# Optimization experiments

Hardware: AMD Instinct MI355X
Metric: run time of the kernel (lower is better)

The kernel has to match this reference:

```python
import jax, jax.numpy as jnp
import numpy as np

N_WIN = 232
T = 8
KERNEL = (2, 2, 2)
STRIDE = (2, 2, 2)
SLOPE = 25.0  # fast_sigmoid surrogate slope


@jax.custom_vjp
def spike(v):
    # heaviside(v) with fast-sigmoid surrogate gradient
    return (v > 0).astype(v.dtype)

def _spike_fwd(v):
    return spike(v), v

def _spike_bwd(v, g):
    return (g / (SLOPE * jnp.abs(v) + 1.0) ** 2,)

spike.defvjp(_spike_fwd, _spike_bwd)


def _avg_pool3d(x, kernel, stride):
    # x: (B, C, D, H, W), VALID pooling
    win = (1, 1) + tuple(kernel)
    st = (1, 1) + tuple(stride)
    s = jax.lax.reduce_window(x, 0.0, jax.lax.add, win, st, 'VALID')
    return s / float(np.prod(kernel))


def setup_inputs() -> dict:
    key = jax.random.key(0)
    ks = jax.random.split(key, 14)
    B, C, H, W = 64, 3, 32, 32
    input_dim, h0, h1, n_cls = 256, 256, 128, 6
    x = jax.random.normal(ks[0], (B, C, N_WIN, H, W), jnp.float32)
    W_in = jax.random.normal(ks[1], (h0, input_dim), jnp.float32) * 0.05
    b_in = jnp.zeros((h0,), jnp.float32)
    W_hid = jax.random.normal(ks[2], (h1, h0), jnp.float32) * 0.05
    b_hid = jnp.zeros((h1,), jnp.float32)
    in_feat = C * h1 * 14  # C * hidden[1] * D'
    W_out = jax.random.normal(ks[3], (n_cls, in_feat), jnp.float32) * 0.05
    b_out = jnp.zeros((n_cls,), jnp.float32)
    beta_in = jax.random.uniform(ks[4], (h0,), jnp.float32)
    thr_in = jax.random.uniform(ks[5], (h0,), jnp.float32)
    beta_hid = jax.random.uniform(ks[6], (h1,), jnp.float32)
    thr_hid = jax.random.uniform(ks[7], (h1,), jnp.float32)
    beta_out = jax.random.uniform(ks[8], (n_cls,), jnp.float32)
    return dict(x=x, W_in=W_in, b_in=b_in, W_hid=W_hid, b_hid=b_hid,
                W_out=W_out, b_out=b_out, beta_in=beta_in, thr_in=thr_in,
                beta_hid=beta_hid, thr_hid=thr_hid, beta_out=beta_out)


def _lif(mem, cur, beta, thr):
    # snntorch Leaky, reset-by-subtract; reset uses detached prev-mem spike
    reset = jax.lax.stop_gradient((mem > thr).astype(mem.dtype))
    mem = jnp.clip(beta, 0.0, 1.0) * mem + cur - reset * thr
    spk = spike(mem - thr)
    return spk, mem


def reference(x, W_in, b_in, W_hid, b_hid, W_out, b_out,
              beta_in, thr_in, beta_hid, thr_hid, beta_out):
    B, C, _, H, W = x.shape
    chunk = N_WIN // T  # 29
    # split depth into T chunks: (T, B, C, chunk, H, W)
    xt = x.reshape(B, C, T, chunk, H, W).transpose(2, 0, 1, 3, 4, 5)
    pooled = jax.vmap(lambda v: _avg_pool3d(v, KERNEL, STRIDE))(xt)  # (T,B,C,D',H',W')
    _, _, _, Dp, Hp, Wp = pooled.shape
    pr = pooled.reshape(T, B, C * Dp, Hp * Wp)
    # fc_in applied to all timesteps at once (recurrence-free)
    cur_in_all = jnp.einsum('tbnf,hf->tbnh', pr, W_in) + b_in  # (T,B,N,h0)

    h0 = W_in.shape[0]
    h1 = W_hid.shape[0]
    n_cls = W_out.shape[0]
    N = C * Dp
    mem_in0 = jnp.zeros((B, N, h0), x.dtype)
    mem_hid0 = jnp.zeros((B, N, h1), x.dtype)
    mem_out0 = jnp.zeros((B, n_cls), x.dtype)

    def step(carry, cur_in):
        mem_in, mem_hid, mem_out = carry
        spk_in, mem_in = _lif(mem_in, cur_in, beta_in, thr_in)
        cur_hid = jnp.einsum('bnh,gh->bng', spk_in, W_hid) + b_hid
        spk_hid, mem_hid = _lif(mem_hid, cur_hid, beta_hid, thr_hid)
        flat = spk_hid.reshape(spk_hid.shape[0], -1)  # (B, N*h1)
        cur_out = flat @ W_out.T + b_out
        spk_out, mem_out = _lif(mem_out, cur_out, beta_out, jnp.float32(1.0))
        return (mem_in, mem_hid, mem_out), spk_out

    _, spk_rec = jax.lax.scan(step, (mem_in0, mem_hid0, mem_out0), cur_in_all)
    return spk_rec  # (T, B, n_classes)
```

## Files before the change

kernel.cpp:

```cpp
#include <hip/hip_runtime.h>

#define T_STEPS 8
#define NROW    42
#define BN      2688
#define H0      256
#define H1      128
#define KFLAT   5376


#define SWA(r)  ((r) + ((r) >> 5) * 4)

__global__ __launch_bounds__(256, 4) void snn_front(
        const float* __restrict__ x,
        const float* __restrict__ Wi,
        const float* __restrict__ bi,
        const float* __restrict__ beti,
        const float* __restrict__ thri,
        const float* __restrict__ Wh,
        const float* __restrict__ bh,
        const float* __restrict__ beth,
        const float* __restrict__ thrh,
        float* __restrict__ spkh) {
    __shared__ float At[16 * 36];
    __shared__ float Bt[16 * 284];
    __shared__ unsigned int S32[256];

    int tid = threadIdx.x;
    int gbase = blockIdx.x * 4;

    int wp = tid & 15;
    int q  = tid >> 4;
    const float* xb0;
    const float* xb1;
    int mloc0 = q * 2, mloc1 = q * 2 + 1;
    {
        int g = gbase + (mloc0 >> 3);
        int t = mloc0 & 7;
        int b = g / 42, r = g - b * 42;
        int c = r / 14, dp = r - c * 14;
        xb0 = x + ((long)b * 712704 + (long)c * 237568
                + (long)(t * 29 + 2 * dp) * 1024 + 2 * wp);
    }
    {
        int g = gbase + (mloc1 >> 3);
        int t = mloc1 & 7;
        int b = g / 42, r = g - b * 42;
        int c = r / 14, dp = r - c * 14;
        xb1 = x + ((long)b * 712704 + (long)c * 237568
                + (long)(t * 29 + 2 * dp) * 1024 + 2 * wp);
    }

    const float* Bp = Wi + (long)tid * 256;
    int bcol = SWA(tid);

    int tm = tid & 3;
    int tn = tid >> 2;
    int ca = tm * 8;
    int cb = SWA(tn * 4);

    float acc[8][4] = {};

    for (int k0 = 0; k0 < 256; k0 += 16) {
        int hp = k0 >> 4;
        const float* p0 = xb0 + hp * 64;
        const float* p1 = xb1 + hp * 64;
        float2 a00 = *(const float2*)(p0);
        float2 a01 = *(const float2*)(p0 + 32);
        float2 a02 = *(const float2*)(p0 + 1024);
        float2 a03 = *(const float2*)(p0 + 1056);
        float2 a10 = *(const float2*)(p1);
        float2 a11 = *(const float2*)(p1 + 32);
        float2 a12 = *(const float2*)(p1 + 1024);
        float2 a13 = *(const float2*)(p1 + 1056);
        float4 w0 = *(const float4*)(Bp + k0);
        float4 w1 = *(const float4*)(Bp + k0 + 4);
        float4 w2 = *(const float4*)(Bp + k0 + 8);
        float4 w3 = *(const float4*)(Bp + k0 + 12);
        __syncthreads();
        float s0 = a00.x + a00.y + a01.x + a01.y + a02.x + a02.y + a03.x + a03.y;
        float s1 = a10.x + a10.y + a11.x + a11.y + a12.x + a12.y + a13.x + a13.y;
        At[wp * 36 + mloc0] = s0 * 0.125f;
        At[wp * 36 + mloc1] = s1 * 0.125f;
        Bt[ 0 * 284 + bcol] = w0.x; Bt[ 1 * 284 + bcol] = w0.y;
        Bt[ 2 * 284 + bcol] = w0.z; Bt[ 3 * 284 + bcol] = w0.w;
        Bt[ 4 * 284 + bcol] = w1.x; Bt[ 5 * 284 + bcol] = w1.y;
        Bt[ 6 * 284 + bcol] = w1.z; Bt[ 7 * 284 + bcol] = w1.w;
        Bt[ 8 * 284 + bcol] = w2.x; Bt[ 9 * 284 + bcol] = w2.y;
        Bt[10 * 284 + bcol] = w2.z; Bt[11 * 284 + bcol] = w2.w;
        Bt[12 * 284 + bcol] = w3.x; Bt[13 * 284 + bcol] = w3.y;
        Bt[14 * 284 + bcol] = w3.z; Bt[15 * 284 + bcol] = w3.w;
        __syncthreads();
#pragma unroll
        for (int k = 0; k < 16; ++k) {
            float4 av0 = *(const float4*)&At[k * 36 + ca];
            float4 av1 = *(const float4*)&At[k * 36 + ca + 4];
            float4 bv  = *(const float4*)&Bt[k * 284 + cb];
            float am[8] = {av0.x, av0.y, av0.z, av0.w, av1.x, av1.y, av1.z, av1.w};
            float bb[4] = {bv.x, bv.y, bv.z, bv.w};
#pragma unroll
            for (int i = 0; i < 8; ++i)
#pragma unroll
                for (int j = 0; j < 4; ++j)
                    acc[i][j] = fmaf(am[i], bb[j], acc[i][j]);
        }
    }

    unsigned int mybyte[4];
#pragma unroll
    for (int j = 0; j < 4; ++j) {
        int h = tn * 4 + j;
        float be = fminf(fmaxf(beti[h], 0.f), 1.f);
        float th = thri[h];
        float bb = bi[h];
        float mem = 0.f;
        unsigned int byte = 0u;
#pragma unroll
        for (int t = 0; t < T_STEPS; ++t) {
            float cur = acc[t][j] + bb;
            float reset = (mem > th) ? th : 0.f;
            mem = be * mem + cur - reset;
            byte |= ((mem - th) > 0.f) ? (1u << t) : 0u;
        }
        mybyte[j] = byte;
    }
    {
        unsigned char* S8 = (unsigned char*)S32;
#pragma unroll
        for (int j = 0; j < 4; ++j)
            S8[(tn * 4 + j) * 4 + tm] = (unsigned char)mybyte[j];
    }
    __syncthreads();

    const float* wrow0 = Wh + (long)(tn * 2) * 256;
    const float* wrow1 = wrow0 + 256;
    int shift = tm * 8;
    float acc2[8][2] = {};

    for (int k0 = 0; k0 < 256; k0 += 16) {
        float4 w00 = *(const float4*)(wrow0 + k0);
        float4 w01 = *(const float4*)(wrow0 + k0 + 4);
        float4 w02 = *(const float4*)(wrow0 + k0 + 8);
        float4 w03 = *(const float4*)(wrow0 + k0 + 12);
        float4 w10 = *(const float4*)(wrow1 + k0);
        float4 w11 = *(const float4*)(wrow1 + k0 + 4);
        float4 w12 = *(const float4*)(wrow1 + k0 + 8);
        float4 w13 = *(const float4*)(wrow1 + k0 + 12);
        float w0a[16] = {w00.x, w00.y, w00.z, w00.w, w01.x, w01.y, w01.z, w01.w,
                         w02.x, w02.y, w02.z, w02.w, w03.x, w03.y, w03.z, w03.w};
        float w1a[16] = {w10.x, w10.y, w10.z, w10.w, w11.x, w11.y, w11.z, w11.w,
                         w12.x, w12.y, w12.z, w12.w, w13.x, w13.y, w13.z, w13.w};
#pragma unroll
        for (int k = 0; k < 16; ++k) {
            unsigned int sw = S32[k0 + k];
#pragma unroll
            for (int i = 0; i < 8; ++i) {
                float am = (float)((sw >> (shift + i)) & 1u);
                acc2[i][0] = fmaf(am, w0a[k], acc2[i][0]);
                acc2[i][1] = fmaf(am, w1a[k], acc2[i][1]);
            }
        }
    }

#pragma unroll
    for (int j = 0; j < 2; ++j) {
        int h = tn * 2 + j;
        float be = fminf(fmaxf(beth[h], 0.f), 1.f);
        float th = thrh[h];
        float bb = bh[h];
        float mem = 0.f;
#pragma unroll
        for (int t = 0; t < T_STEPS; ++t) {
            float cur = acc2[t][j] + bb;
            float reset = (mem > th) ? th : 0.f;
            mem = be * mem + cur - reset;
            acc2[t][j] = ((mem - th) > 0.f) ? 1.f : 0.f;
        }
    }
    int rbase = blockIdx.x * 32 + tm * 8;
#pragma unroll
    for (int t = 0; t < T_STEPS; ++t) {
        float2 o = {acc2[t][0], acc2[t][1]};
        *(float2*)&spkh[(long)(rbase + t) * 128 + tn * 2] = o;
    }
}

__global__ __launch_bounds__(512) void out_fused(const float* __restrict__ spkh,
                                                 const float* __restrict__ W_out,
                                                 const float* __restrict__ b_out,
                                                 const float* __restrict__ beta_out,
                                                 float* __restrict__ out) {
    __shared__ float part[2][256][8];
    __shared__ float curs[8][8];
    int b = blockIdx.x;
    int grp = threadIdx.x >> 8;
    int tid = threadIdx.x & 255;

    for (int tr = 0; tr < 4; ++tr) {
        int t = tr * 2 + grp;
        float acc[6] = {0.f, 0.f, 0.f, 0.f, 0.f, 0.f};
        for (int j = tid; j < KFLAT; j += 256) {
            int n = j >> 7, h = j & 127;
            float s = spkh[((long)(b * NROW + n) * 8 + t) * 128 + h];
#pragma unroll
            for (int c = 0; c < 6; ++c)
                acc[c] = fmaf(s, W_out[c * KFLAT + j], acc[c]);
        }
#pragma unroll
        for (int c = 0; c < 6; ++c) part[grp][tid][c] = acc[c];
        __syncthreads();
        for (int off = 128; off > 0; off >>= 1) {
            if (tid < off) {
#pragma unroll
                for (int c = 0; c < 6; ++c)
                    part[grp][tid][c] += part[grp][tid + off][c];
            }
            __syncthreads();
        }
        if (tid < 6) curs[t][tid] = part[grp][0][tid] + b_out[tid];
        __syncthreads();
    }

    if (threadIdx.x < 6) {
        int cls = threadIdx.x;
        float be = fminf(fmaxf(beta_out[cls], 0.f), 1.f);
        float mem = 0.f;
#pragma unroll
        for (int t = 0; t < T_STEPS; ++t) {
            float cur = curs[t][cls];
            float reset = (mem > 1.f) ? 1.f : 0.f;
            mem = be * mem + cur - reset;
            out[t * 384 + b * 6 + cls] = ((mem - 1.f) > 0.f) ? 1.f : 0.f;
        }
    }
}

extern "C" void kernel_launch(void* const* d_in, const int* in_sizes, int n_in,
                              void* d_out, int out_size, void* d_ws, size_t ws_size,
                              hipStream_t stream) {
    (void)in_sizes; (void)n_in; (void)out_size; (void)ws_size;
    const float* x        = (const float*)d_in[0];
    const float* W_in     = (const float*)d_in[1];
    const float* b_in     = (const float*)d_in[2];
    const float* W_hid    = (const float*)d_in[3];
    const float* b_hid    = (const float*)d_in[4];
    const float* W_out    = (const float*)d_in[5];
    const float* b_out    = (const float*)d_in[6];
    const float* beta_in  = (const float*)d_in[7];
    const float* thr_in   = (const float*)d_in[8];
    const float* beta_hid = (const float*)d_in[9];
    const float* thr_hid  = (const float*)d_in[10];
    const float* beta_out = (const float*)d_in[11];
    float* out = (float*)d_out;

    float* buf0 = (float*)d_ws;

    snn_front<<<672, 256, 0, stream>>>(x, W_in, b_in, beta_in, thr_in,
                                       W_hid, b_hid, beta_hid, thr_hid, buf0);
    out_fused<<<64, 512, 0, stream>>>(buf0, W_out, b_out, beta_out, out);
}
```

Baseline: 370.8 us.

## Double-buffer front GEMM shared tiles and split output GEMM from LIF

Double-buffers the shared-memory A/B tiles in the front kernel. Global loads for the next K-chunk are issued before the FMA loop on the current buffer, which removes one barrier per iteration and hides load latency. Occupancy is lowered from 4 to 3 blocks per CU to fit the larger shared footprint. The output stage is split into a 512-block GEMM kernel that writes cur_out to workspace, followed by a tiny LIF kernel. This gives more parallelism than 64 blocks, at the cost of an extra launch.

```diff
diff --git a/kernel.cpp b/kernel.cpp
--- a/kernel.cpp
+++ b/kernel.cpp
@@ -10,7 +10,7 @@
 
 #define SWA(r)  ((r) + ((r) >> 5) * 4)
 
-__global__ __launch_bounds__(256, 4) void snn_front(
+__global__ __launch_bounds__(256, 3) void snn_front(
         const float* __restrict__ x,
         const float* __restrict__ Wi,
         const float* __restrict__ bi,
@@ -21,8 +21,8 @@
         const float* __restrict__ beth,
         const float* __restrict__ thrh,
         float* __restrict__ spkh) {
-    __shared__ float At[16 * 36];
-    __shared__ float Bt[16 * 284];
+    __shared__ float At[2 * 576];
+    __shared__ float Bt[2 * 4544];
     __shared__ unsigned int S32[256];
 
     int tid = threadIdx.x;
@@ -59,51 +59,69 @@
     int cb = SWA(tn * 4);
 
     float acc[8][4] = {};
-
-    for (int k0 = 0; k0 < 256; k0 += 16) {
-        int hp = k0 >> 4;
-        const float* p0 = xb0 + hp * 64;
-        const float* p1 = xb1 + hp * 64;
-        float2 a00 = *(const float2*)(p0);
-        float2 a01 = *(const float2*)(p0 + 32);
-        float2 a02 = *(const float2*)(p0 + 1024);
-        float2 a03 = *(const float2*)(p0 + 1056);
-        float2 a10 = *(const float2*)(p1);
-        float2 a11 = *(const float2*)(p1 + 32);
-        float2 a12 = *(const float2*)(p1 + 1024);
-        float2 a13 = *(const float2*)(p1 + 1056);
-        float4 w0 = *(const float4*)(Bp + k0);
-        float4 w1 = *(const float4*)(Bp + k0 + 4);
-        float4 w2 = *(const float4*)(Bp + k0 + 8);
-        float4 w3 = *(const float4*)(Bp + k0 + 12);
+    float2 a00, a01, a02, a03, a10, a11, a12, a13;
+    float4 w0, w1, w2, w3;
+
+#define ISSUE(hp) {                                                        \
+    const float* p0 = xb0 + (hp) * 64;                                     \
+    const float* p1 = xb1 + (hp) * 64;                                     \
+    a00 = *(const float2*)(p0);        a01 = *(const float2*)(p0 + 32);    \
+    a02 = *(const float2*)(p0 + 1024); a03 = *(const float2*)(p0 + 1056);  \
+    a10 = *(const float2*)(p1);        a11 = *(const float2*)(p1 + 32);    \
+    a12 = *(const float2*)(p1 + 1024); a13 = *(const float2*)(p1 + 1056);  \
+    const float* Bk = Bp + (hp) * 16;                                      \
+    w0 = *(const float4*)(Bk);     w1 = *(const float4*)(Bk + 4);          \
+    w2 = *(const float4*)(Bk + 8); w3 = *(const float4*)(Bk + 12); }
+
+#define STAGE(bufi) {                                                      \
+    float s0 = a00.x + a00.y + a01.x + a01.y + a02.x + a02.y + a03.x + a03.y; \
+    float s1 = a10.x + a10.y + a11.x + a11.y + a12.x + a12.y + a13.x + a13.y; \
+    float* At_ = At + (bufi) * 576;                                        \
+    float* Bt_ = Bt + (bufi) * 4544;                                       \
+    At_[wp * 36 + mloc0] = s0 * 0.125f;                                    \
+    At_[wp * 36 + mloc1] = s1 * 0.125f;                                    \
+    Bt_[ 0 * 284 + bcol] = w0.x; Bt_[ 1 * 284 + bcol] = w0.y;              \
+    Bt_[ 2 * 284 + bcol] = w0.z; Bt_[ 3 * 284 + bcol] = w0.w;              \
+    Bt_[ 4 * 284 + bcol] = w1.x; Bt_[ 5 * 284 + bcol] = w1.y;              \
+    Bt_[ 6 * 284 + bcol] = w1.z; Bt_[ 7 * 284 + bcol] = w1.w;              \
+    Bt_[ 8 * 284 + bcol] = w2.x; Bt_[ 9 * 284 + bcol] = w2.y;              \
+    Bt_[10 * 284 + bcol] = w2.z; Bt_[11 * 284 + bcol] = w2.w;              \
+    Bt_[12 * 284 + bcol] = w3.x; Bt_[13 * 284 + bcol] = w3.y;              \
+    Bt_[14 * 284 + bcol] = w3.z; Bt_[15 * 284 + bcol] = w3.w; }
+
+#define FMACHUNK(bufi) {                                                   \
+    const float* At_ = At + (bufi) * 576;                                  \
+    const float* Bt_ = Bt + (bufi) * 4544;                                 \
+    _Pragma("unroll")                                                      \
+    for (int k = 0; k < 16; ++k) {                                         \
+        float4 av0 = *(const float4*)&At_[k * 36 + ca];                    \
+        float4 av1 = *(const float4*)&At_[k * 36 + ca + 4];                \
+        float4 bv  = *(const float4*)&Bt_[k * 284 + cb];                   \
+        float am[8] = {av0.x, av0.y, av0.z, av0.w,                         \
+                       av1.x, av1.y, av1.z, av1.w};                        \
+        float bb[4] = {bv.x, bv.y, bv.z, bv.w};                            \
+        _Pragma("unroll")                                                  \
+        for (int i2 = 0; i2 < 8; ++i2)                                     \
+            _Pragma("unroll")                                              \
+            for (int j2 = 0; j2 < 4; ++j2)                                 \
+                acc[i2][j2] = fmaf(am[i2], bb[j2], acc[i2][j2]);           \
+    } }
+
+    ISSUE(0);
+    STAGE(0);
+#pragma unroll 1
+    for (int i = 0; i < 15; ++i) {
+        ISSUE(i + 1);
         __syncthreads();
-        float s0 = a00.x + a00.y + a01.x + a01.y + a02.x + a02.y + a03.x + a03.y;
-        float s1 = a10.x + a10.y + a11.x + a11.y + a12.x + a12.y + a13.x + a13.y;
-        At[wp * 36 + mloc0] = s0 * 0.125f;
-        At[wp * 36 + mloc1] = s1 * 0.125f;
-        Bt[ 0 * 284 + bcol] = w0.x; Bt[ 1 * 284 + bcol] = w0.y;
-        Bt[ 2 * 284 + bcol] = w0.z; Bt[ 3 * 284 + bcol] = w0.w;
-        Bt[ 4 * 284 + bcol] = w1.x; Bt[ 5 * 284 + bcol] = w1.y;
-        Bt[ 6 * 284 + bcol] = w1.z; Bt[ 7 * 284 + bcol] = w1.w;
-        Bt[ 8 * 284 + bcol] = w2.x; Bt[ 9 * 284 + bcol] = w2.y;
-        Bt[10 * 284 + bcol] = w2.z; Bt[11 * 284 + bcol] = w2.w;
-        Bt[12 * 284 + bcol] = w3.x; Bt[13 * 284 + bcol] = w3.y;
-        Bt[14 * 284 + bcol] = w3.z; Bt[15 * 284 + bcol] = w3.w;
-        __syncthreads();
-#pragma unroll
-        for (int k = 0; k < 16; ++k) {
-            float4 av0 = *(const float4*)&At[k * 36 + ca];
-            float4 av1 = *(const float4*)&At[k * 36 + ca + 4];
-            float4 bv  = *(const float4*)&Bt[k * 284 + cb];
-            float am[8] = {av0.x, av0.y, av0.z, av0.w, av1.x, av1.y, av1.z, av1.w};
-            float bb[4] = {bv.x, bv.y, bv.z, bv.w};
-#pragma unroll
-            for (int i = 0; i < 8; ++i)
-#pragma unroll
-                for (int j = 0; j < 4; ++j)
-                    acc[i][j] = fmaf(am[i], bb[j], acc[i][j]);
-        }
-    }
+        FMACHUNK(i & 1);
+        STAGE((i + 1) & 1);
+    }
+    __syncthreads();
+    FMACHUNK(1);
+
+#undef ISSUE
+#undef STAGE
+#undef FMACHUNK
 
     unsigned int mybyte[4];
 #pragma unroll
@@ -184,53 +202,49 @@
     }
 }
 
-__global__ __launch_bounds__(512) void out_fused(const float* __restrict__ spkh,
-                                                 const float* __restrict__ W_out,
-                                                 const float* __restrict__ b_out,
-                                                 const float* __restrict__ beta_out,
-                                                 float* __restrict__ out) {
-    __shared__ float part[2][256][8];
-    __shared__ float curs[8][8];
-    int b = blockIdx.x;
-    int grp = threadIdx.x >> 8;
-    int tid = threadIdx.x & 255;
-
-    for (int tr = 0; tr < 4; ++tr) {
-        int t = tr * 2 + grp;
-        float acc[6] = {0.f, 0.f, 0.f, 0.f, 0.f, 0.f};
-        for (int j = tid; j < KFLAT; j += 256) {
-            int n = j >> 7, h = j & 127;
-            float s = spkh[((long)(b * NROW + n) * 8 + t) * 128 + h];
-#pragma unroll
-            for (int c = 0; c < 6; ++c)
-                acc[c] = fmaf(s, W_out[c * KFLAT + j], acc[c]);
-        }
-#pragma unroll
-        for (int c = 0; c < 6; ++c) part[grp][tid][c] = acc[c];
+__global__ __launch_bounds__(256) void out_gemm(const float* __restrict__ spkh,
+                                                const float* __restrict__ W_out,
+                                                const float* __restrict__ b_out,
+                                                float* __restrict__ cur_out) {
+    __shared__ float part[256][8];
+    int row = blockIdx.x;
+    int t = row >> 6, b = row & 63;
+    int tid = threadIdx.x;
+    float acc[6] = {0.f, 0.f, 0.f, 0.f, 0.f, 0.f};
+    for (int j = tid; j < KFLAT; j += 256) {
+        int n = j >> 7, h = j & 127;
+        float s = spkh[((long)(b * NROW + n) * 8 + t) * 128 + h];
+#pragma unroll
+        for (int c = 0; c < 6; ++c)
+            acc[c] = fmaf(s, W_out[c * KFLAT + j], acc[c]);
+    }
+#pragma unroll
+    for (int c = 0; c < 6; ++c) part[tid][c] = acc[c];
+    __syncthreads();
+    for (int off = 128; off > 0; off >>= 1) {
+        if (tid < off) {
+#pragma unroll
+            for (int c = 0; c < 6; ++c) part[tid][c] += part[tid + off][c];
+        }
         __syncthreads();
-        for (int off = 128; off > 0; off >>= 1) {
-            if (tid < off) {
-#pragma unroll
-                for (int c = 0; c < 6; ++c)
-                    part[grp][tid][c] += part[grp][tid + off][c];
-            }
-            __syncthreads();
-        }
-        if (tid < 6) curs[t][tid] = part[grp][0][tid] + b_out[tid];
-        __syncthreads();
-    }
-
-    if (threadIdx.x < 6) {
-        int cls = threadIdx.x;
-        float be = fminf(fmaxf(beta_out[cls], 0.f), 1.f);
-        float mem = 0.f;
-#pragma unroll
-        for (int t = 0; t < T_STEPS; ++t) {
-            float cur = curs[t][cls];
-            float reset = (mem > 1.f) ? 1.f : 0.f;
-            mem = be * mem + cur - reset;
-            out[t * 384 + b * 6 + cls] = ((mem - 1.f) > 0.f) ? 1.f : 0.f;
-        }
+    }
+    if (tid < 6) cur_out[row * 6 + tid] = part[0][tid] + b_out[tid];
+}
+
+__global__ void lif_out_kernel(const float* __restrict__ cur_out,
+                               const float* __restrict__ beta_out,
+                               float* __restrict__ out) {
+    int j = threadIdx.x;
+    if (j >= 384) return;
+    int cls = j % 6;
+    float be = fminf(fmaxf(beta_out[cls], 0.f), 1.f);
+    float mem = 0.f;
+#pragma unroll
+    for (int t = 0; t < T_STEPS; ++t) {
+        float cur = cur_out[t * 384 + j];
+        float reset = (mem > 1.f) ? 1.f : 0.f;
+        mem = be * mem + cur - reset;
+        out[t * 384 + j] = ((mem - 1.f) > 0.f) ? 1.f : 0.f;
     }
 }
 
@@ -253,8 +267,10 @@
     float* out = (float*)d_out;
 
     float* buf0 = (float*)d_ws;
+    float* curo = buf0 + 2752512;
 
     snn_front<<<672, 256, 0, stream>>>(x, W_in, b_in, beta_in, thr_in,
                                        W_hid, b_hid, beta_hid, thr_hid, buf0);
-    out_fused<<<64, 512, 0, stream>>>(buf0, W_out, b_out, beta_out, out);
-}
+    out_gemm<<<512, 256, 0, stream>>>(buf0, W_out, b_out, curo);
+    lif_out_kernel<<<1, 384, 0, stream>>>(curo, beta_out, out);
+}
```

Result: faster. 353.2 us (-4.8%).

## Split output GEMM across batch-time blocks with last-block LIF via atomic counter

Applied to the files above, without the earlier changes.

Replaces the 64-block output kernel, which looped over timesteps inside each block, with a 512-block kernel that gives each (t,b) row its own block. Partial currents go to workspace, and the last block per batch item, found with an atomic counter, runs the output LIF recurrence. This raises parallelism in the small tail kernel at the cost of atomics, fences and a counter reset inside the front kernel.

```diff
diff --git a/kernel.cpp b/kernel.cpp
--- a/kernel.cpp
+++ b/kernel.cpp
@@ -20,12 +20,14 @@
         const float* __restrict__ bh,
         const float* __restrict__ beth,
         const float* __restrict__ thrh,
-        float* __restrict__ spkh) {
+        float* __restrict__ spkh,
+        int* __restrict__ cnt) {
     __shared__ float At[16 * 36];
     __shared__ float Bt[16 * 284];
     __shared__ unsigned int S32[256];
 
     int tid = threadIdx.x;
+    if (blockIdx.x == 0 && tid < 64) cnt[tid] = 0;
     int gbase = blockIdx.x * 4;
 
     int wp = tid & 15;
@@ -184,52 +186,55 @@
     }
 }
 
-__global__ __launch_bounds__(512) void out_fused(const float* __restrict__ spkh,
-                                                 const float* __restrict__ W_out,
-                                                 const float* __restrict__ b_out,
-                                                 const float* __restrict__ beta_out,
-                                                 float* __restrict__ out) {
-    __shared__ float part[2][256][8];
-    __shared__ float curs[8][8];
-    int b = blockIdx.x;
-    int grp = threadIdx.x >> 8;
-    int tid = threadIdx.x & 255;
-
-    for (int tr = 0; tr < 4; ++tr) {
-        int t = tr * 2 + grp;
-        float acc[6] = {0.f, 0.f, 0.f, 0.f, 0.f, 0.f};
-        for (int j = tid; j < KFLAT; j += 256) {
-            int n = j >> 7, h = j & 127;
-            float s = spkh[((long)(b * NROW + n) * 8 + t) * 128 + h];
-#pragma unroll
-            for (int c = 0; c < 6; ++c)
-                acc[c] = fmaf(s, W_out[c * KFLAT + j], acc[c]);
-        }
-#pragma unroll
-        for (int c = 0; c < 6; ++c) part[grp][tid][c] = acc[c];
+__global__ __launch_bounds__(256) void out_gemm(const float* __restrict__ spkh,
+                                                const float* __restrict__ W_out,
+                                                const float* __restrict__ b_out,
+                                                const float* __restrict__ beta_out,
+                                                float* __restrict__ cur_out,
+                                                int* __restrict__ cnt,
+                                                float* __restrict__ out) {
+    __shared__ float part[256][8];
+    __shared__ int amlast;
+    int row = blockIdx.x;
+    int t = row >> 6, b = row & 63;
+    int tid = threadIdx.x;
+    float acc[6] = {0.f, 0.f, 0.f, 0.f, 0.f, 0.f};
+    for (int j = tid; j < KFLAT; j += 256) {
+        int n = j >> 7, h = j & 127;
+        float s = spkh[((long)(b * NROW + n) * 8 + t) * 128 + h];
+#pragma unroll
+        for (int c = 0; c < 6; ++c)
+            acc[c] = fmaf(s, W_out[c * KFLAT + j], acc[c]);
+    }
+#pragma unroll
+    for (int c = 0; c < 6; ++c) part[tid][c] = acc[c];
+    __syncthreads();
+    for (int off = 128; off > 0; off >>= 1) {
+        if (tid < off) {
+#pragma unroll
+            for (int c = 0; c < 6; ++c) part[tid][c] += part[tid + off][c];
+        }
         __syncthreads();
-        for (int off = 128; off > 0; off >>= 1) {
-            if (tid < off) {
-#pragma unroll
-                for (int c = 0; c < 6; ++c)
-                    part[grp][tid][c] += part[grp][tid + off][c];
+    }
+    if (tid < 6) cur_out[row * 6 + tid] = part[0][tid] + b_out[tid];
+
+    __threadfence();
+    __syncthreads();
+    if (tid == 0) amlast = (atomicAdd(&cnt[b], 1) == 7) ? 1 : 0;
+    __syncthreads();
+    if (amlast) {
+        __threadfence();
+        if (tid < 6) {
+            int cls = tid;
+            float be = fminf(fmaxf(beta_out[cls], 0.f), 1.f);
+            float mem = 0.f;
+#pragma unroll
+            for (int tt = 0; tt < T_STEPS; ++tt) {
+                float cur = cur_out[tt * 384 + b * 6 + cls];
+                float reset = (mem > 1.f) ? 1.f : 0.f;
+                mem = be * mem + cur - reset;
+                out[tt * 384 + b * 6 + cls] = ((mem - 1.f) > 0.f) ? 1.f : 0.f;
             }
-            __syncthreads();
-        }
-        if (tid < 6) curs[t][tid] = part[grp][0][tid] + b_out[tid];
-        __syncthreads();
-    }
-
-    if (threadIdx.x < 6) {
-        int cls = threadIdx.x;
-        float be = fminf(fmaxf(beta_out[cls], 0.f), 1.f);
-        float mem = 0.f;
-#pragma unroll
-        for (int t = 0; t < T_STEPS; ++t) {
-            float cur = curs[t][cls];
-            float reset = (mem > 1.f) ? 1.f : 0.f;
-            mem = be * mem + cur - reset;
-            out[t * 384 + b * 6 + cls] = ((mem - 1.f) > 0.f) ? 1.f : 0.f;
         }
     }
 }
@@ -253,8 +258,12 @@
     float* out = (float*)d_out;
 
     float* buf0 = (float*)d_ws;
+    float* curo = buf0 + 2752512;
+    int*   cnt  = (int*)(curo + 3072);
 
     snn_front<<<672, 256, 0, stream>>>(x, W_in, b_in, beta_in, thr_in,
-                                       W_hid, b_hid, beta_hid, thr_hid, buf0);
-    out_fused<<<64, 512, 0, stream>>>(buf0, W_out, b_out, beta_out, out);
+                                       W_hid, b_hid, beta_hid, thr_hid,
+                                       buf0, cnt);
+    out_gemm<<<512, 256, 0, stream>>>(buf0, W_out, b_out, beta_out,
+                                      curo, cnt, out);
 }
```

Result: slower. 383.1 us (+3.3%).
